# Kernel tuning notes

Measured on AMD Instinct MI355X. Metric: run time of the kernel, lower is better.

The kernel has to match this reference:

```python
import jax, jax.numpy as jnp
import numpy as np

NC = 256        # number of query contexts
N_ANS = 500000  # answer bank size
N_CTX = 500000  # context bank size
DIM = 128       # embedding dim
K = 32          # topk width


def setup_inputs() -> dict:
    key = jax.random.key(0)
    k1, k2, k3 = jax.random.split(key, 3)
    contexts = jax.random.normal(k1, (NC, DIM), dtype=jnp.float32)
    enc_ans = jax.random.normal(k2, (N_ANS, DIM), dtype=jnp.float32)
    enc_ctx = jax.random.normal(k3, (N_CTX, DIM), dtype=jnp.float32)
    return {"contexts": contexts, "enc_ans": enc_ans, "enc_ctx": enc_ctx, "k": K}


def reference(contexts, enc_ans, enc_ctx, k):
    # Hop 1: find k most similar contexts in the context bank.
    sims_ctx = jnp.einsum('qd,nd->qn', contexts, enc_ctx)          # [nc, N_ctx]
    _, c_ixs = jax.lax.top_k(sims_ctx, k)                          # [nc, k]
    # Gather neighbor contexts and average them (vectorized form of the
    # original per-row list comprehension + cat).
    new_contexts = enc_ctx[c_ixs].mean(axis=1)                     # [nc, dim]
    # Hop 2: rank answers against the averaged neighbor contexts.
    sims_ans = jnp.einsum('qd,nd->qn', new_contexts, enc_ans)      # [nc, N_ans]
    _, ixs = jax.lax.top_k(sims_ans, k)                            # [nc, k] int
    return ixs
```

## Files before the change

kernel.cpp:

```cpp
#include <hip/hip_runtime.h>
#include <hip/hip_bf16.h>
#include <float.h>


#define TILE 64
#define KSEL 32
#define TSEL 64
#define NT_MAX 7936
#define EQCAP 256
#define POOLCAP 256
#define SGRID 512

typedef __attribute__((ext_vector_type(8))) short s16x8;
typedef __attribute__((ext_vector_type(4))) float f32x4;

__device__ __forceinline__ unsigned f2key(float f) {
  unsigned u = __float_as_uint(f);
  return (u & 0x80000000u) ? ~u : (u | 0x80000000u);
}

__device__ __forceinline__ s16x8 pack_bf16(float4 a, float4 b) {
  union { s16x8 v; unsigned u[4]; } r;
  r.u[0] = (__float_as_uint(a.y) & 0xffff0000u) | (__float_as_uint(a.x) >> 16);
  r.u[1] = (__float_as_uint(a.w) & 0xffff0000u) | (__float_as_uint(a.z) >> 16);
  r.u[2] = (__float_as_uint(b.y) & 0xffff0000u) | (__float_as_uint(b.x) >> 16);
  r.u[3] = (__float_as_uint(b.w) & 0xffff0000u) | (__float_as_uint(b.z) >> 16);
  return r.v;
}

__device__ __forceinline__ void async_copy16(const float* g, float* l) {
  __builtin_amdgcn_global_load_lds(
      (const __attribute__((address_space(1))) unsigned int*)g,
      (__attribute__((address_space(3))) unsigned int*)l, 16, 0, 0);
}

__global__ void cvt_a_kernel(const float* __restrict__ A,
                             unsigned short* __restrict__ Abf, int nelem) {
  int i = blockIdx.x * 256 + threadIdx.x;
  if (i < nelem) Abf[i] = (unsigned short)(__float_as_uint(A[i]) >> 16);
}

__global__ __launch_bounds__(256) void score_mfma_kernel(
    const unsigned short* __restrict__ Abf,
    const float* __restrict__ bank,
    int n, int NT,
    float* __restrict__ tilemax) {
  __shared__ float bsm[2][TILE * 128];
  const int t = threadIdx.x;
  const int wave = t >> 6;
  const int lane = t & 63;
  const int quad = lane >> 4;
  const int lh   = lane & 15;
  const int q0   = wave * 64;
  const float4 z4 = make_float4(0.f, 0.f, 0.f, 0.f);

  const int per = (NT + (int)gridDim.x - 1) / (int)gridDim.x;
  const int tt0 = blockIdx.x * per;
  const int tt1 = (tt0 + per < NT) ? tt0 + per : NT;
  if (tt0 >= tt1) return;

  s16x8 afr[4][4];
#pragma unroll
  for (int qb = 0; qb < 4; ++qb)
#pragma unroll
    for (int k = 0; k < 4; ++k)
      afr[qb][k] = *(const s16x8*)(Abf + (size_t)(q0 + qb * 16 + lh) * 128 + k * 32 + quad * 8);

  auto stage = [&](int bb, int tile) {
    if (tile * TILE + TILE <= n) {
      const float* gsrc = bank + (size_t)tile * (TILE * 128);
#pragma unroll
      for (int i = 0; i < 8; ++i) {
        const int seg = wave * 8 + i;
        async_copy16(gsrc + seg * 256 + lane * 4, &bsm[bb][seg * 256]);
      }
    } else {
#pragma unroll
      for (int i = 0; i < 8; ++i) {
        int idx = t + i * 256;
        int row = idx >> 5, c4 = idx & 31;
        int g = tile * TILE + row;
        float4 v = (g < n) ? *(const float4*)(bank + (size_t)g * 128 + c4 * 4) : z4;
        *(float4*)(&bsm[bb][row * 128 + c4 * 4]) = v;
      }
    }
  };

  int c = tt0, cur = 0;
  stage(0, c);
  __syncthreads();

  while (true) {
    if (c + 1 < tt1) stage(cur ^ 1, c + 1);

    f32x4 vmax[4];
#pragma unroll
    for (int qb = 0; qb < 4; ++qb)
      vmax[qb] = f32x4{-FLT_MAX, -FLT_MAX, -FLT_MAX, -FLT_MAX};

#pragma unroll
    for (int cbi = 0; cbi < 4; ++cbi) {
      const float* bp = &bsm[cur][(cbi * 16 + lh) * 128 + quad * 8];
      s16x8 bfr[4];
#pragma unroll
      for (int k = 0; k < 4; ++k) {
        float4 fa = *(const float4*)(bp + k * 32);
        float4 fb = *(const float4*)(bp + k * 32 + 4);
        bfr[k] = pack_bf16(fa, fb);
      }
#pragma unroll
      for (int qb = 0; qb < 4; ++qb) {
        f32x4 acc = {0.f, 0.f, 0.f, 0.f};
#pragma unroll
        for (int k = 0; k < 4; ++k)
          acc = __builtin_amdgcn_mfma_f32_16x16x32_bf16(afr[qb][k], bfr[k], acc, 0, 0, 0);
#pragma unroll
        for (int r = 0; r < 4; ++r) vmax[qb][r] = fmaxf(vmax[qb][r], acc[r]);
      }
    }

#pragma unroll
    for (int qb = 0; qb < 4; ++qb) {
#pragma unroll
      for (int r = 0; r < 4; ++r) {
        float v = vmax[qb][r];
        v = fmaxf(v, __shfl_xor(v, 1, 64));
        v = fmaxf(v, __shfl_xor(v, 2, 64));
        v = fmaxf(v, __shfl_xor(v, 4, 64));
        v = fmaxf(v, __shfl_xor(v, 8, 64));
        if (lh == 0)
          tilemax[(size_t)(q0 + qb * 16 + quad * 4 + r) * NT + c] = v;
      }
    }

    if (c + 1 >= tt1) break;
    __syncthreads();
    cur ^= 1;
    ++c;
  }
}

struct RadixSM {
  int hist[4][256];
  int ss[256];
  unsigned prefix;
  int t;
};

__device__ __forceinline__ void radix_select(const unsigned* __restrict__ key,
                                             int N, int target, int tid,
                                             RadixSM* sm,
                                             unsigned* outK, int* out_tres) {
  if (tid == 0) { sm->prefix = 0u; sm->t = target; }
  __syncthreads();
  const int wv = tid >> 6;
  for (int r = 0; r < 4; ++r) {
    const int shift = 24 - 8 * r;
    const unsigned kmask = (r == 0) ? 0u : (0xFFFFFFFFu << (32 - 8 * r));
    sm->hist[0][tid] = 0; sm->hist[1][tid] = 0;
    sm->hist[2][tid] = 0; sm->hist[3][tid] = 0;
    __syncthreads();
    const unsigned pref = sm->prefix;
    for (int i = tid; i < N; i += 256) {
      unsigned k = key[i];
      if ((k & kmask) == pref) atomicAdd(&sm->hist[wv][(k >> shift) & 255], 1);
    }
    __syncthreads();
    int v = sm->hist[0][tid] + sm->hist[1][tid] + sm->hist[2][tid] + sm->hist[3][tid];
    sm->ss[tid] = v;
    __syncthreads();
    for (int d = 1; d < 256; d <<= 1) {
      int add = (tid + d < 256) ? sm->ss[tid + d] : 0;
      __syncthreads();
      v += add;
      sm->ss[tid] = v;
      __syncthreads();
    }
    const int tcur = sm->t;
    const int hiCnt = (tid < 255) ? sm->ss[tid + 1] : 0;
    __syncthreads();
    if (v >= tcur && hiCnt < tcur) {
      sm->prefix = pref | ((unsigned)tid << shift);
      sm->t = tcur - hiCnt;
    }
    __syncthreads();
  }
  *outK = sm->prefix;
  *out_tres = sm->t;
}

__global__ __launch_bounds__(256) void select_tiles_kernel(
    const float* __restrict__ tilemax,
    int NT,
    int* __restrict__ sel_g) {
  const int q = blockIdx.x;
  const int t = threadIdx.x;
  __shared__ unsigned key[NT_MAX];
  __shared__ RadixSM rsm;
  __shared__ int n_hi, n_eq;
  __shared__ int eqs[EQCAP];

  if (t < TSEL) sel_g[(size_t)q * TSEL + t] = 0;

  for (int i = t; i < NT; i += 256)
    key[i] = f2key(tilemax[(size_t)q * NT + i]);
  if (t == 0) { n_hi = 0; n_eq = 0; }
  __syncthreads();

  unsigned K; int tres;
  radix_select(key, NT, TSEL, t, &rsm, &K, &tres);

  for (int i = t; i < NT; i += 256) {
    unsigned k = key[i];
    if (k > K) {
      int p = atomicAdd(&n_hi, 1);
      if (p < TSEL) sel_g[(size_t)q * TSEL + p] = i;
    } else if (k == K) {
      int p = atomicAdd(&n_eq, 1);
      if (p < EQCAP) eqs[p] = i;
    }
  }
  __syncthreads();
  const int nh = n_hi < TSEL ? n_hi : TSEL;
  const int ne = n_eq < EQCAP ? n_eq : EQCAP;
  if (t < ne) {
    int mine = eqs[t];
    int rank = 0;
    for (int j = 0; j < ne; ++j) rank += (eqs[j] < mine) ? 1 : 0;
    if (rank < tres && nh + rank < TSEL)
      sel_g[(size_t)q * TSEL + nh + rank] = mine;
  }
}

__global__ __launch_bounds__(256) void rescore_kernel(
    const float* __restrict__ A,
    const float* __restrict__ bank,
    int n,
    const int* __restrict__ sel_g,
    float* __restrict__ sc) {
  const int q = blockIdx.x >> 4;
  const int part = blockIdx.x & 15;
  const int t = threadIdx.x;
  __shared__ __align__(16) float aq[128];
  __shared__ int tiles[4];
  if (t < 128) aq[t] = A[(size_t)q * 128 + t];
  if (t >= 128 && t < 132)
    tiles[t - 128] = sel_g[(size_t)q * TSEL + part * 4 + (t - 128)];
  __syncthreads();

  const int tile = tiles[t >> 6];
  const int cand = tile * TILE + (t & 63);
  float s = -FLT_MAX;
  if (cand >= 0 && cand < n) {
    const float* row = bank + (size_t)cand * 128;
    float a0 = 0.f, a1 = 0.f;
#pragma unroll
    for (int i = 0; i < 128; i += 8) {
      float4 b0 = *(const float4*)(row + i);
      float4 b1 = *(const float4*)(row + i + 4);
      float4 x0 = *(const float4*)(aq + i);
      float4 x1 = *(const float4*)(aq + i + 4);
      a0 += x0.x * b0.x + x0.y * b0.y + x0.z * b0.z + x0.w * b0.w;
      a1 += x1.x * b1.x + x1.y * b1.y + x1.z * b1.z + x1.w * b1.w;
    }
    s = a0 + a1;
  }
  sc[(size_t)q * (TSEL * TILE) + part * 256 + t] = s;
}

__global__ __launch_bounds__(256) void topk_kernel(
    const int* __restrict__ sel_g,
    const float* __restrict__ sc,
    int* __restrict__ out) {
  const int q = blockIdx.x;
  const int t = threadIdx.x;
  __shared__ unsigned key[TSEL * TILE];
  __shared__ int sel_s[TSEL];
  __shared__ RadixSM rsm;
  __shared__ int n_pool;
  __shared__ int poolc[POOLCAP];
  __shared__ unsigned poolk[POOLCAP];

  if (t < TSEL) sel_s[t] = sel_g[(size_t)q * TSEL + t];
  for (int j = t; j < TSEL * TILE; j += 256)
    key[j] = f2key(sc[(size_t)q * (TSEL * TILE) + j]);
  if (t == 0) n_pool = 0;
  __syncthreads();

  unsigned K; int tres;
  radix_select(key, TSEL * TILE, KSEL, t, &rsm, &K, &tres);
  (void)tres;

  for (int j = t; j < TSEL * TILE; j += 256) {
    unsigned k = key[j];
    if (k >= K) {
      int p = atomicAdd(&n_pool, 1);
      if (p < POOLCAP) {
        poolk[p] = k;
        poolc[p] = sel_s[j >> 6] * TILE + (j & 63);
      }
    }
  }
  __syncthreads();
  const int np = n_pool < POOLCAP ? n_pool : POOLCAP;
  if (t < np) {
    unsigned mk = poolk[t];
    int mc = poolc[t];
    int rank = 0;
    for (int j = 0; j < np; ++j) {
      unsigned k = poolk[j];
      int c = poolc[j];
      rank += (k > mk || (k == mk && c < mc)) ? 1 : 0;
    }
    if (rank < KSEL) out[(size_t)q * KSEL + rank] = mc;
  }
}

__global__ void mean_gather_kernel(
    const float* __restrict__ bank,
    const int* __restrict__ ixs,
    float* __restrict__ outA,
    unsigned short* __restrict__ outAbf) {
  const int q = blockIdx.x;
  const int d = threadIdx.x;
  float s = 0.f;
  for (int j = 0; j < KSEL; ++j)
    s += bank[(size_t)ixs[q * KSEL + j] * 128 + d];
  s *= (1.0f / 32.0f);
  outA[(size_t)q * 128 + d] = s;
  outAbf[(size_t)q * 128 + d] = (unsigned short)(__float_as_uint(s) >> 16);
}

extern "C" void kernel_launch(void* const* d_in, const int* in_sizes, int n_in,
                              void* d_out, int out_size, void* d_ws, size_t ws_size,
                              hipStream_t stream) {
  const float* contexts = (const float*)d_in[0];
  const float* enc_ans  = (const float*)d_in[1];
  const float* enc_ctx  = (const float*)d_in[2];
  const int n_ans = in_sizes[1] / 128;
  const int n_ctx = in_sizes[2] / 128;
  const int NT_ctx = (n_ctx + TILE - 1) / TILE;
  const int NT_ans = (n_ans + TILE - 1) / TILE;
  const int NT_big = NT_ctx > NT_ans ? NT_ctx : NT_ans;

  char* ws = (char*)d_ws;
  size_t off = 0;
  float* tilemax = (float*)(ws + off);
  off += ((size_t)256 * NT_big * 4 + 255) & ~(size_t)255;
  int* c_ixs = (int*)(ws + off);
  off += ((size_t)256 * KSEL * 4 + 255) & ~(size_t)255;
  float* new_ctx = (float*)(ws + off);
  off += ((size_t)256 * 128 * 4 + 255) & ~(size_t)255;
  unsigned short* Abf1 = (unsigned short*)(ws + off);
  off += ((size_t)256 * 128 * 2 + 255) & ~(size_t)255;
  unsigned short* Abf2 = (unsigned short*)(ws + off);

  float* sc = tilemax;
  int* sel_g = (int*)Abf1;

  cvt_a_kernel<<<128, 256, 0, stream>>>(contexts, Abf1, 256 * 128);
  score_mfma_kernel<<<SGRID, 256, 0, stream>>>(Abf1, enc_ctx, n_ctx, NT_ctx, tilemax);
  select_tiles_kernel<<<256, 256, 0, stream>>>(tilemax, NT_ctx, sel_g);
  rescore_kernel<<<4096, 256, 0, stream>>>(contexts, enc_ctx, n_ctx, sel_g, sc);
  topk_kernel<<<256, 256, 0, stream>>>(sel_g, sc, c_ixs);
  mean_gather_kernel<<<256, 128, 0, stream>>>(enc_ctx, c_ixs, new_ctx, Abf2);

  score_mfma_kernel<<<SGRID, 256, 0, stream>>>(Abf2, enc_ans, n_ans, NT_ans, tilemax);
  select_tiles_kernel<<<256, 256, 0, stream>>>(tilemax, NT_ans, sel_g);
  rescore_kernel<<<4096, 256, 0, stream>>>(new_ctx, enc_ans, n_ans, sel_g, sc);
  topk_kernel<<<256, 256, 0, stream>>>(sel_g, sc, (int*)d_out);
}
```

Measured before the change: 909.4 us.

## XOR-swizzle shared-memory tile layout and stage rescore tiles through LDS

Applies an XOR swizzle to the LDS tile layout in the MFMA scoring kernel, permuting the source addresses of the async global-to-LDS copies so that strided row reads from shared memory avoid bank conflicts. The rescore kernel is reworked so each block handles one selected tile: it async-copies the 64x128 tile into swizzled LDS, then 64 threads compute the dot products from LDS instead of reading rows directly from global memory. This targets LDS bank conflicts in the hot scoring loop and uncoalesced per-thread row reads in rescoring. In exchange, three quarters of the threads in each rescore block sit idle during compute, and four times as many blocks are launched.

```diff
diff --git a/kernel.cpp b/kernel.cpp
--- a/kernel.cpp
+++ b/kernel.cpp
@@ -33,6 +33,7 @@
       (const __attribute__((address_space(1))) unsigned int*)g,
       (__attribute__((address_space(3))) unsigned int*)l, 16, 0, 0);
 }
+
 
 __global__ void cvt_a_kernel(const float* __restrict__ A,
                              unsigned short* __restrict__ Abf, int nelem) {
@@ -72,7 +73,8 @@
 #pragma unroll
       for (int i = 0; i < 8; ++i) {
         const int seg = wave * 8 + i;
-        async_copy16(gsrc + seg * 256 + lane * 4, &bsm[bb][seg * 256]);
+        const int lsw = lane ^ ((2 * seg + (lane >> 5)) & 7);
+        async_copy16(gsrc + seg * 256 + lsw * 4, &bsm[bb][seg * 256]);
       }
     } else {
 #pragma unroll
@@ -81,7 +83,7 @@
         int row = idx >> 5, c4 = idx & 31;
         int g = tile * TILE + row;
         float4 v = (g < n) ? *(const float4*)(bank + (size_t)g * 128 + c4 * 4) : z4;
-        *(float4*)(&bsm[bb][row * 128 + c4 * 4]) = v;
+        *(float4*)(&bsm[bb][(row * 128 + c4 * 4) ^ ((row & 7) << 2)]) = v;
       }
     }
   };
@@ -90,6 +92,8 @@
   stage(0, c);
   __syncthreads();
 
+  const int sw = (lh & 7) << 2;
+
   while (true) {
     if (c + 1 < tt1) stage(cur ^ 1, c + 1);
 
@@ -100,12 +104,12 @@
 
 #pragma unroll
     for (int cbi = 0; cbi < 4; ++cbi) {
-      const float* bp = &bsm[cur][(cbi * 16 + lh) * 128 + quad * 8];
+      const int rbase = (cbi * 16 + lh) * 128 + quad * 8;
       s16x8 bfr[4];
 #pragma unroll
       for (int k = 0; k < 4; ++k) {
-        float4 fa = *(const float4*)(bp + k * 32);
-        float4 fb = *(const float4*)(bp + k * 32 + 4);
+        float4 fa = *(const float4*)(&bsm[cur][(rbase + k * 32) ^ sw]);
+        float4 fb = *(const float4*)(&bsm[cur][(rbase + k * 32 + 4) ^ sw]);
         bfr[k] = pack_bf16(fa, fb);
       }
 #pragma unroll
@@ -238,34 +242,58 @@
     int n,
     const int* __restrict__ sel_g,
     float* __restrict__ sc) {
-  const int q = blockIdx.x >> 4;
-  const int part = blockIdx.x & 15;
+  const int q   = blockIdx.x >> 6;
+  const int tix = blockIdx.x & 63;
   const int t = threadIdx.x;
+  const int wave = t >> 6;
+  const int lane = t & 63;
+  __shared__ float bsm[TILE * 128];
   __shared__ __align__(16) float aq[128];
-  __shared__ int tiles[4];
+  const float4 z4 = make_float4(0.f, 0.f, 0.f, 0.f);
+
+  const int tile = sel_g[(size_t)q * TSEL + tix];
+
+  if (tile * TILE + TILE <= n) {
+    const float* gsrc = bank + (size_t)tile * (TILE * 128);
+#pragma unroll
+    for (int i = 0; i < 8; ++i) {
+      const int seg = wave * 8 + i;
+      const int lsw = lane ^ ((2 * seg + (lane >> 5)) & 7);
+      async_copy16(gsrc + seg * 256 + lsw * 4, &bsm[seg * 256]);
+    }
+  } else {
+#pragma unroll
+    for (int i = 0; i < 8; ++i) {
+      int idx = t + i * 256;
+      int row = idx >> 5, c4 = idx & 31;
+      int g = tile * TILE + row;
+      float4 v = (g < n) ? *(const float4*)(bank + (size_t)g * 128 + c4 * 4) : z4;
+      *(float4*)(&bsm[(row * 128 + c4 * 4) ^ ((row & 7) << 2)]) = v;
+    }
+  }
   if (t < 128) aq[t] = A[(size_t)q * 128 + t];
-  if (t >= 128 && t < 132)
-    tiles[t - 128] = sel_g[(size_t)q * TSEL + part * 4 + (t - 128)];
-  __syncthreads();
-
-  const int tile = tiles[t >> 6];
-  const int cand = tile * TILE + (t & 63);
-  float s = -FLT_MAX;
-  if (cand >= 0 && cand < n) {
-    const float* row = bank + (size_t)cand * 128;
-    float a0 = 0.f, a1 = 0.f;
-#pragma unroll
-    for (int i = 0; i < 128; i += 8) {
-      float4 b0 = *(const float4*)(row + i);
-      float4 b1 = *(const float4*)(row + i + 4);
-      float4 x0 = *(const float4*)(aq + i);
-      float4 x1 = *(const float4*)(aq + i + 4);
-      a0 += x0.x * b0.x + x0.y * b0.y + x0.z * b0.z + x0.w * b0.w;
-      a1 += x1.x * b1.x + x1.y * b1.y + x1.z * b1.z + x1.w * b1.w;
-    }
-    s = a0 + a1;
-  }
-  sc[(size_t)q * (TSEL * TILE) + part * 256 + t] = s;
+  __syncthreads();
+
+  if (t < TILE) {
+    const int cand = tile * TILE + t;
+    float s = -FLT_MAX;
+    if (cand < n) {
+      const int sw = (t & 7) << 2;
+      const int rb = t * 128;
+      float a0 = 0.f, a1 = 0.f;
+#pragma unroll
+      for (int i = 0; i < 128; i += 8) {
+        float4 b0 = *(const float4*)(&bsm[(rb + i) ^ sw]);
+        float4 b1 = *(const float4*)(&bsm[(rb + i + 4) ^ sw]);
+        float4 x0 = *(const float4*)(aq + i);
+        float4 x1 = *(const float4*)(aq + i + 4);
+        a0 += x0.x * b0.x + x0.y * b0.y + x0.z * b0.z + x0.w * b0.w;
+        a1 += x1.x * b1.x + x1.y * b1.y + x1.z * b1.z + x1.w * b1.w;
+      }
+      s = a0 + a1;
+    }
+    sc[(size_t)q * (TSEL * TILE) + tix * TILE + t] = s;
+  }
 }
 
 __global__ __launch_bounds__(256) void topk_kernel(
@@ -361,12 +389,12 @@
   cvt_a_kernel<<<128, 256, 0, stream>>>(contexts, Abf1, 256 * 128);
   score_mfma_kernel<<<SGRID, 256, 0, stream>>>(Abf1, enc_ctx, n_ctx, NT_ctx, tilemax);
   select_tiles_kernel<<<256, 256, 0, stream>>>(tilemax, NT_ctx, sel_g);
-  rescore_kernel<<<4096, 256, 0, stream>>>(contexts, enc_ctx, n_ctx, sel_g, sc);
+  rescore_kernel<<<256 * TSEL, 256, 0, stream>>>(contexts, enc_ctx, n_ctx, sel_g, sc);
   topk_kernel<<<256, 256, 0, stream>>>(sel_g, sc, c_ixs);
   mean_gather_kernel<<<256, 128, 0, stream>>>(enc_ctx, c_ixs, new_ctx, Abf2);
 
   score_mfma_kernel<<<SGRID, 256, 0, stream>>>(Abf2, enc_ans, n_ans, NT_ans, tilemax);
   select_tiles_kernel<<<256, 256, 0, stream>>>(tilemax, NT_ans, sel_g);
-  rescore_kernel<<<4096, 256, 0, stream>>>(new_ctx, enc_ans, n_ans, sel_g, sc);
+  rescore_kernel<<<256 * TSEL, 256, 0, stream>>>(new_ctx, enc_ans, n_ans, sel_g, sc);
   topk_kernel<<<256, 256, 0, stream>>>(sel_g, sc, (int*)d_out);
 }
```

Result: no change. 918.1 us (+1.0%).
